# Kernel optimization log

Measured on AMD Instinct MI355X. Metric: run time of the kernel, lower is better.

Reference implementation:

```python
import jax, jax.numpy as jnp
import numpy as np

K = 20          # neighbors
EPS = 1e-5      # BatchNorm eps
SLOPE = 0.2     # LeakyReLU negative slope


def setup_inputs() -> dict:
    key = jax.random.key(0)
    ks = jax.random.split(key, 6)
    B, C, N, O = 8, 3, 4096, 64
    x = jax.random.normal(ks[0], (B, C, N), dtype=jnp.float32)
    W = jax.random.normal(ks[1], (O, 2 * C), dtype=jnp.float32) * 0.1  # conv1x1 weight, bias=False
    gamma = 1.0 + 0.1 * jax.random.normal(ks[2], (O,), dtype=jnp.float32)
    beta = 0.1 * jax.random.normal(ks[3], (O,), dtype=jnp.float32)
    mean = 0.1 * jax.random.normal(ks[4], (O,), dtype=jnp.float32)
    var = jax.random.uniform(ks[5], (O,), dtype=jnp.float32, minval=0.5, maxval=1.5)
    return {"x": x, "W": W, "gamma": gamma, "beta": beta, "mean": mean, "var": var}


def reference(x, W, gamma, beta, mean, var):
    # x: [B, C, N]
    B, C, N = x.shape
    xt = jnp.swapaxes(x, 1, 2)                                   # [B, N, C]
    xx = jnp.sum(x * x, axis=1)                                  # [B, N]
    pd = 2.0 * jnp.einsum('bnc,bmc->bnm', xt, xt) - xx[:, :, None] - xx[:, None, :]
    _, idx = jax.lax.top_k(pd, K)                                # [B, N, K] nearest neighbors
    # gather neighbor features per batch
    feat = jax.vmap(lambda f, i: f[i])(xt, idx)                  # [B, N, K, C]
    center = xt[:, :, None, :]                                   # [B, N, 1, C]
    edge = jnp.concatenate(
        [feat - center, jnp.broadcast_to(center, feat.shape)], axis=-1)  # [B, N, K, 2C]
    # 1x1 conv == channel matmul
    y = jnp.einsum('bnkc,oc->bnko', edge, W)                     # [B, N, K, O]
    inv = gamma / jnp.sqrt(var + EPS)                            # fused inference BatchNorm
    y = y * inv + (beta - mean * inv)
    y = jnp.where(y >= 0, y, SLOPE * y)                          # LeakyReLU(0.2)
    y = jnp.max(y, axis=2)                                       # max over k -> [B, N, O]
    return jnp.swapaxes(y, 1, 2)                                 # [B, O, N]
```

## Files before the change

kernel.cpp:

```cpp
#include <hip/hip_runtime.h>
#include <math.h>

#define NPTS 4096
#define KNN  20
#define NOUT 64
#define WPB  8
#define QPW  4
#define QBLK (WPB * QPW)
#define BLKT (WPB * 64)
#define PCAP 96
#define HALF 1536

__device__ __forceinline__ unsigned ord32(float f) {
    unsigned u = __float_as_uint(f);
    int m = ((int)u) >> 31;
    return u ^ ((unsigned)m | 0x80000000u);
}
__device__ __forceinline__ float iord32(unsigned r) {
    unsigned u = (r & 0x80000000u) ? (r ^ 0x80000000u) : ~r;
    return __uint_as_float(u);
}
__device__ __forceinline__ int mbcnt64(unsigned long long m) {
    return __builtin_amdgcn_mbcnt_hi((unsigned)(m >> 32),
           __builtin_amdgcn_mbcnt_lo((unsigned)m, 0));
}

__global__ __launch_bounds__(256) void pack_kernel(const float* __restrict__ x,
                                                   float4* __restrict__ xq) {
    const int i = blockIdx.x * 256 + threadIdx.x;
    const int b = i >> 12, j = i & (NPTS - 1);
    const float* xb = x + (size_t)b * 3 * NPTS;
    const float a0 = xb[j], a1 = xb[NPTS + j], a2 = xb[2 * NPTS + j];
    xq[i] = make_float4(a0, a1, a2, -fmaf(a0, a0, fmaf(a1, a1, a2 * a2)));
}

__global__ __launch_bounds__(BLKT, 6) void edgeconv_kernel(
    const float4* __restrict__ xq,
    const float* __restrict__ Wm,
    const float* __restrict__ gamma,
    const float* __restrict__ beta,
    const float* __restrict__ mean,
    const float* __restrict__ var,
    float* __restrict__ out)
{
    const int bid = blockIdx.x;
    const int b   = bid >> 7;
    const int n0  = (bid & 127) * QBLK;
    const int t    = threadIdx.x;
    const int lane = t & 63;
    const int w    = t >> 6;

    __shared__ float4 tile[HALF];
    __shared__ unsigned long long pool[QBLK * PCAP];
    __shared__ int cnt[QBLK];

    const float4* xqb = xq + (size_t)b * NPTS;

    if (lane < QPW) cnt[QPW * w + lane] = 0;

    const int na = __builtin_amdgcn_readfirstlane(n0 + QPW * w);
    float q0[QPW], q1[QPW], q2[QPW];
    #pragma unroll
    for (int q = 0; q < QPW; ++q) {
        const float4 pv = xqb[na + q];
        q0[q] = 2.f * pv.x; q1[q] = 2.f * pv.y; q2[q] = 2.f * pv.z;
    }

    float vm0[QPW], vm1[QPW];
    #pragma unroll
    for (int q = 0; q < QPW; ++q) { vm0[q] = -INFINITY; vm1[q] = -INFINITY; }

    #pragma unroll
    for (int k2 = 0; k2 < HALF / BLKT; ++k2) {
        const int c = t + k2 * BLKT;
        const float4 cc = xqb[c];
        tile[c] = cc;
        #pragma unroll
        for (int q = 0; q < QPW; ++q) {
            const float e = fmaf(q0[q], cc.x, fmaf(q1[q], cc.y, fmaf(q2[q], cc.z, cc.w)));
            vm1[q] = fmaxf(vm1[q], e);
        }
    }

    #pragma unroll
    for (int g = 0; g < 10; ++g) {
        float4 cc[4];
        #pragma unroll
        for (int u = 0; u < 4; ++u) cc[u] = xqb[HALF + (g * 4 + u) * 64 + lane];
        #pragma unroll
        for (int u = 0; u < 4; ++u) {
            #pragma unroll
            for (int q = 0; q < QPW; ++q) {
                const float e = fmaf(q0[q], cc[u].x, fmaf(q1[q], cc[u].y, fmaf(q2[q], cc[u].z, cc[u].w)));
                if (g < 5) vm0[q] = fmaxf(vm0[q], e);
                else       vm1[q] = fmaxf(vm1[q], e);
            }
        }
    }

    float Tf[QPW];
    #pragma unroll
    for (int q = 0; q < QPW; ++q) {
        const unsigned h0 = ord32(vm0[q]) >> 16;
        const unsigned h1 = ord32(vm1[q]) >> 16;
        unsigned K = 0;
        #pragma unroll
        for (int bit = 15; bit >= 0; --bit) {
            const unsigned p = K | (1u << bit);
            const int c = __popcll(__ballot(h0 >= p)) + __popcll(__ballot(h1 >= p));
            if (c >= KNN) K = p;
        }
        Tf[q] = iord32(K << 16);
    }

    __syncthreads();

    const int invl = (NPTS - 1) - lane;

    #pragma unroll
    for (int g = 0; g < 6; ++g) {
        float4 cc[4];
        #pragma unroll
        for (int u = 0; u < 4; ++u) cc[u] = tile[(g * 4 + u) * 64 + lane];
        #pragma unroll
        for (int u = 0; u < 4; ++u) {
            const unsigned tag = (unsigned)(invl - (g * 4 + u) * 64);
            #pragma unroll
            for (int q = 0; q < QPW; ++q) {
                const float e = fmaf(q0[q], cc[u].x, fmaf(q1[q], cc[u].y, fmaf(q2[q], cc[u].z, cc[u].w)));
                if (e >= Tf[q]) {
                    const int pos = atomicAdd(&cnt[QPW * w + q], 1);
                    if (pos < PCAP)
                        pool[(QPW * w + q) * PCAP + pos] =
                            ((unsigned long long)ord32(e) << 32) | tag;
                }
            }
        }
    }

    #pragma unroll
    for (int g = 0; g < 10; ++g) {
        float4 cc[4];
        #pragma unroll
        for (int u = 0; u < 4; ++u) cc[u] = xqb[HALF + (g * 4 + u) * 64 + lane];
        #pragma unroll
        for (int u = 0; u < 4; ++u) {
            const unsigned tag = (unsigned)(invl - HALF - (g * 4 + u) * 64);
            #pragma unroll
            for (int q = 0; q < QPW; ++q) {
                const float e = fmaf(q0[q], cc[u].x, fmaf(q1[q], cc[u].y, fmaf(q2[q], cc[u].z, cc[u].w)));
                if (e >= Tf[q]) {
                    const int pos = atomicAdd(&cnt[QPW * w + q], 1);
                    if (pos < PCAP)
                        pool[(QPW * w + q) * PCAP + pos] =
                            ((unsigned long long)ord32(e) << 32) | tag;
                }
            }
        }
    }

    unsigned myidx[QPW];
    #pragma unroll
    for (int q = 0; q < QPW; ++q) {
        const int pr = QPW * w + q;
        unsigned long long* pl = pool + (size_t)pr * PCAP;
        int cw = __builtin_amdgcn_readfirstlane(cnt[pr]);
        if (cw > PCAP) cw = PCAP;

        const unsigned long long e0 = (lane < cw) ? pl[lane] : 0ull;
        const unsigned long long e1 = (lane + 64 < cw) ? pl[lane + 64] : 0ull;
        const unsigned k0 = (unsigned)(e0 >> 32), t0 = (unsigned)e0;
        const unsigned k1 = (unsigned)(e1 >> 32), t1 = (unsigned)e1;

        unsigned K = 0;
        #pragma unroll
        for (int bit = 31; bit >= 0; --bit) {
            const unsigned p = K | (1u << bit);
            const int c = __popcll(__ballot(k0 >= p)) + __popcll(__ballot(k1 >= p));
            if (c >= KNN) K = p;
        }

        unsigned long long g0 = __ballot(k0 > K);
        unsigned long long g1 = __ballot(k1 > K);
        const int m = __popcll(g0) + __popcll(g1);
        unsigned long long s0 = __ballot(k0 == K);
        unsigned long long s1 = __ballot(k1 == K);
        const int r = KNN - m;
        if (__popcll(s0) + __popcll(s1) > r) {
            unsigned TT = 0;
            #pragma unroll
            for (int bit = 11; bit >= 0; --bit) {
                const unsigned p = TT | (1u << bit);
                const int c = __popcll(__ballot(k0 == K && t0 >= p)) +
                              __popcll(__ballot(k1 == K && t1 >= p));
                if (c >= r) TT = p;
            }
            s0 = __ballot(k0 == K && t0 >= TT);
            s1 = __ballot(k1 == K && t1 >= TT);
        }

        unsigned* idxq = (unsigned*)pl;
        if ((g0 >> lane) & 1) idxq[mbcnt64(g0)] = t0;
        if ((g1 >> lane) & 1) idxq[__popcll(g0) + mbcnt64(g1)] = t1;
        if ((s0 >> lane) & 1) idxq[m + mbcnt64(s0)] = t0;
        if ((s1 >> lane) & 1) idxq[m + __popcll(s0) + mbcnt64(s1)] = t1;
        myidx[q] = idxq[(lane < KNN) ? lane : 0];
    }

    __syncthreads();

    const int o = lane;
    const float iv   = gamma[o] / sqrtf(var[o] + 1e-5f);
    const float bias = beta[o] - mean[o] * iv;
    const float* Wr = Wm + o * 6;
    const float w0p = Wr[0] * iv, w1p = Wr[1] * iv, w2p = Wr[2] * iv;
    const float w3p = Wr[3] * iv, w4p = Wr[4] * iv, w5p = Wr[5] * iv;

    float* outT = (float*)pool;
    #pragma unroll
    for (int q = 0; q < QPW; ++q) {
        const float4 pv = xqb[na + q];
        const float basep = fmaf(w3p, pv.x, fmaf(w4p, pv.y, fmaf(w5p, pv.z, bias)));
        const float base2 = basep - fmaf(w0p, pv.x, fmaf(w1p, pv.y, w2p * pv.z));
        float best = -INFINITY;
        #pragma unroll
        for (int k = 0; k < KNN; ++k) {
            const int lk = __builtin_amdgcn_readlane((int)myidx[q], k);
            const int gi = __builtin_amdgcn_readfirstlane((NPTS - 1) - lk);
            const float4 f = xqb[gi];
            float y = fmaf(w0p, f.x, fmaf(w1p, f.y, fmaf(w2p, f.z, base2)));
            y = fmaxf(y, 0.2f * y);
            best = fmaxf(best, y);
        }
        outT[o * (QBLK + 1) + QPW * w + q] = best;
    }
    __syncthreads();

    {
        const int oo = t >> 3, seg = t & 7;
        const int sb = oo * (QBLK + 1) + seg * 4;
        float4 vv;
        vv.x = outT[sb + 0]; vv.y = outT[sb + 1];
        vv.z = outT[sb + 2]; vv.w = outT[sb + 3];
        *(float4*)(out + ((size_t)b * NOUT + oo) * NPTS + n0 + seg * 4) = vv;
    }
}

extern "C" void kernel_launch(void* const* d_in, const int* in_sizes, int n_in,
                              void* d_out, int out_size, void* d_ws, size_t ws_size,
                              hipStream_t stream) {
    const float* x     = (const float*)d_in[0];
    const float* Wm    = (const float*)d_in[1];
    const float* gamma = (const float*)d_in[2];
    const float* beta  = (const float*)d_in[3];
    const float* mean  = (const float*)d_in[4];
    const float* var   = (const float*)d_in[5];
    float* out = (float*)d_out;
    float4* xq = (float4*)d_ws;

    const int B = in_sizes[0] / (3 * NPTS);
    pack_kernel<<<B * NPTS / 256, 256, 0, stream>>>(x, xq);
    const int nblocks = B * (NPTS / QBLK);
    edgeconv_kernel<<<nblocks, BLKT, 0, stream>>>(xq, Wm, gamma, beta, mean, var, out);
}
```

Measured before the change: 136.6 us.

## Drop LDS candidate tile, halve block to 4 waves, stream candidates from global

Removes the shared-memory tile that cached the first 1536 candidate points, so both scan passes now read every candidate directly from global memory (expected to hit L1/L2). Blocks shrink from 8 to 4 waves (32 to 16 queries per block, twice as many blocks), and the per-query pool capacity rises from 96 to 128 entries. This removes a barrier and frees LDS for occupancy, at the cost of more global/L2 load traffic for the second pass and less reuse of each fetched candidate across waves. The output write mapping is adjusted for the smaller block.

```diff
diff --git a/kernel.cpp b/kernel.cpp
--- a/kernel.cpp
+++ b/kernel.cpp
@@ -4,12 +4,11 @@
 #define NPTS 4096
 #define KNN  20
 #define NOUT 64
-#define WPB  8
+#define WPB  4
 #define QPW  4
 #define QBLK (WPB * QPW)
 #define BLKT (WPB * 64)
-#define PCAP 96
-#define HALF 1536
+#define PCAP 128
 
 __device__ __forceinline__ unsigned ord32(float f) {
     unsigned u = __float_as_uint(f);
@@ -44,13 +43,12 @@
     float* __restrict__ out)
 {
     const int bid = blockIdx.x;
-    const int b   = bid >> 7;
-    const int n0  = (bid & 127) * QBLK;
+    const int b   = bid >> 8;
+    const int n0  = (bid & 255) * QBLK;
     const int t    = threadIdx.x;
     const int lane = t & 63;
     const int w    = t >> 6;
 
-    __shared__ float4 tile[HALF];
     __shared__ unsigned long long pool[QBLK * PCAP];
     __shared__ int cnt[QBLK];
 
@@ -69,30 +67,17 @@
     float vm0[QPW], vm1[QPW];
     #pragma unroll
     for (int q = 0; q < QPW; ++q) { vm0[q] = -INFINITY; vm1[q] = -INFINITY; }
-
-    #pragma unroll
-    for (int k2 = 0; k2 < HALF / BLKT; ++k2) {
-        const int c = t + k2 * BLKT;
-        const float4 cc = xqb[c];
-        tile[c] = cc;
-        #pragma unroll
-        for (int q = 0; q < QPW; ++q) {
-            const float e = fmaf(q0[q], cc.x, fmaf(q1[q], cc.y, fmaf(q2[q], cc.z, cc.w)));
-            vm1[q] = fmaxf(vm1[q], e);
-        }
-    }
-
-    #pragma unroll
-    for (int g = 0; g < 10; ++g) {
+    #pragma unroll
+    for (int g = 0; g < NPTS / 256; ++g) {
         float4 cc[4];
         #pragma unroll
-        for (int u = 0; u < 4; ++u) cc[u] = xqb[HALF + (g * 4 + u) * 64 + lane];
+        for (int u = 0; u < 4; ++u) cc[u] = xqb[(g * 4 + u) * 64 + lane];
         #pragma unroll
         for (int u = 0; u < 4; ++u) {
             #pragma unroll
             for (int q = 0; q < QPW; ++q) {
                 const float e = fmaf(q0[q], cc[u].x, fmaf(q1[q], cc[u].y, fmaf(q2[q], cc[u].z, cc[u].w)));
-                if (g < 5) vm0[q] = fmaxf(vm0[q], e);
+                if (g < 8) vm0[q] = fmaxf(vm0[q], e);
                 else       vm1[q] = fmaxf(vm1[q], e);
             }
         }
@@ -113,39 +98,16 @@
         Tf[q] = iord32(K << 16);
     }
 
-    __syncthreads();
-
     const int invl = (NPTS - 1) - lane;
 
     #pragma unroll
-    for (int g = 0; g < 6; ++g) {
+    for (int g = 0; g < NPTS / 256; ++g) {
         float4 cc[4];
         #pragma unroll
-        for (int u = 0; u < 4; ++u) cc[u] = tile[(g * 4 + u) * 64 + lane];
+        for (int u = 0; u < 4; ++u) cc[u] = xqb[(g * 4 + u) * 64 + lane];
         #pragma unroll
         for (int u = 0; u < 4; ++u) {
             const unsigned tag = (unsigned)(invl - (g * 4 + u) * 64);
-            #pragma unroll
-            for (int q = 0; q < QPW; ++q) {
-                const float e = fmaf(q0[q], cc[u].x, fmaf(q1[q], cc[u].y, fmaf(q2[q], cc[u].z, cc[u].w)));
-                if (e >= Tf[q]) {
-                    const int pos = atomicAdd(&cnt[QPW * w + q], 1);
-                    if (pos < PCAP)
-                        pool[(QPW * w + q) * PCAP + pos] =
-                            ((unsigned long long)ord32(e) << 32) | tag;
-                }
-            }
-        }
-    }
-
-    #pragma unroll
-    for (int g = 0; g < 10; ++g) {
-        float4 cc[4];
-        #pragma unroll
-        for (int u = 0; u < 4; ++u) cc[u] = xqb[HALF + (g * 4 + u) * 64 + lane];
-        #pragma unroll
-        for (int u = 0; u < 4; ++u) {
-            const unsigned tag = (unsigned)(invl - HALF - (g * 4 + u) * 64);
             #pragma unroll
             for (int q = 0; q < QPW; ++q) {
                 const float e = fmaf(q0[q], cc[u].x, fmaf(q1[q], cc[u].y, fmaf(q2[q], cc[u].z, cc[u].w)));
@@ -237,7 +199,7 @@
     __syncthreads();
 
     {
-        const int oo = t >> 3, seg = t & 7;
+        const int oo = t >> 2, seg = t & 3;
         const int sb = oo * (QBLK + 1) + seg * 4;
         float4 vv;
         vv.x = outT[sb + 0]; vv.y = outT[sb + 1];
```

After: 136.2 us. Within noise of the previous version (-0.3%).
